# Optimization experiments

Hardware: AMD Instinct MI355X
Metric: run time of the kernel (lower is better)

## Reference

```python
import jax, jax.numpy as jnp
import numpy as np

F, H, K, T, IT, S = 128, 128, 768, 4, 2, 57  # feat, hidden, max_child, edge types, iters, num_sem


def setup_inputs() -> dict:
    key = jax.random.key(0)
    ks = jax.random.split(key, 12)

    def w(k, shape):
        fan = shape[0] if len(shape) == 2 else shape[1]
        return jax.random.normal(k, shape, jnp.float32) * fan ** -0.5

    return {
        "parent_feature": jax.random.normal(ks[0], (1, F), jnp.float32),
        "W_parent": w(ks[1], (F, H * K)), "b_parent": jnp.zeros((H * K,), jnp.float32),
        "W_exists": w(ks[2], (H, 1)), "b_exists": jnp.zeros((1,), jnp.float32),
        "W_edge_lat": w(ks[3], (2 * H, H)), "b_edge_lat": jnp.zeros((H,), jnp.float32),
        "W_edge_ex": w(ks[4], (T, H)), "b_edge_ex": jnp.zeros((T,), jnp.float32),
        "W_ne": w(ks[5], (IT, 2 * H, H)), "b_ne": jnp.zeros((IT, H), jnp.float32),
        "W_child": w(ks[6], (H * (IT + 1), H)), "b_child": jnp.zeros((H,), jnp.float32),
        "W_sem": w(ks[7], (H, S)), "b_sem": jnp.zeros((S,), jnp.float32),
        "W_child2": w(ks[8], (H, F)), "b_child2": jnp.zeros((F,), jnp.float32),
    }


def reference(parent_feature, W_parent, b_parent, W_exists, b_exists,
              W_edge_lat, b_edge_lat, W_edge_ex, b_edge_ex,
              W_ne, b_ne, W_child, b_child, W_sem, b_sem, W_child2, b_child2):
    # parent -> K child latents
    x = jax.nn.relu(parent_feature @ W_parent + b_parent)  # [1, K*H]
    cf = x.reshape(1, K, H)                                 # child feats
    exists_logits = cf @ W_exists + b_exists                # [1, K, 1]

    # pairwise edge latents [1, K, K, 2H] -> [1, K, K, H]
    pair0 = jnp.concatenate([
        jnp.broadcast_to(cf[:, :, None, :], (1, K, K, H)),
        jnp.broadcast_to(cf[:, None, :, :], (1, K, K, H))], axis=3)
    elat = jax.nn.relu(pair0 @ W_edge_lat + b_edge_lat)
    edge_logits = jnp.einsum('bijh,th->bijt', elat, W_edge_ex) + b_edge_ex  # [1,K,K,T]

    # fixed edge set: existing edges between existing nodes (dense mask form)
    exists = exists_logits[0, :, 0] > 0                     # [K]
    emask = jnp.any(edge_logits[0] > 0, axis=-1) & exists[:, None] & exists[None, :]
    any_edge = jnp.any(emask)

    feats = [cf]
    for i in range(IT):
        c = cf[0]                                           # [K, H]
        pair = jnp.concatenate([
            jnp.broadcast_to(c[:, None, :], (K, K, H)),
            jnp.broadcast_to(c[None, :, :], (K, K, H))], axis=2)
        msg = jax.nn.relu(pair @ W_ne[i] + b_ne[i])         # [K, K, H], >= 0
        msg = jnp.where(emask[:, :, None], msg, 0.0)
        # scatter_max with zeros-initialized out == max over masked neighbors (msg >= 0)
        new_cf = msg.max(axis=1)[None]                      # [1, K, H]
        cf = jnp.where(any_edge, new_cf, cf)                # no edges -> feats unchanged
        feats.append(cf)

    h = jnp.concatenate(feats, axis=2).reshape(K, H * (IT + 1))
    h = jax.nn.relu(h @ W_child + b_child)                  # [K, H]
    sem_logits = (h @ W_sem + b_sem).reshape(1, K, S)
    child_out = jax.nn.relu(h @ W_child2 + b_child2).reshape(1, K, F)
    return child_out, sem_logits, exists_logits, edge_logits
```

## Files before the change

### kernel.cpp

```cpp
#include <hip/hip_runtime.h>
#include <hip/hip_bf16.h>


#define NK 768
#define NH 128
#define NCF 98304

typedef float v2f __attribute__((ext_vector_type(2)));

__global__ __launch_bounds__(512) void k_pd(const float* __restrict__ pf,
    const float* __restrict__ Wp, const float* __restrict__ bp,
    const float* __restrict__ Wexi, const float* __restrict__ bexi,
    const float* __restrict__ Wel, const float* __restrict__ bel,
    const float* __restrict__ Wne, const float* __restrict__ Wee,
    float* __restrict__ cf0g, float* __restrict__ exO,
    float* __restrict__ A_T, float* __restrict__ BT,
    float* __restrict__ A0, float* __restrict__ B0,
    float* __restrict__ WeeT, unsigned int* __restrict__ flag)
{
    __shared__ float s_pf[128];
    __shared__ float s_cf0[2][128];
    __shared__ __align__(16) char s_scr[16384];
    int t = threadIdx.x;
    int b = blockIdx.x;
    int k0 = 2 * b;
    if (t < 128) s_pf[t] = pf[t];
    if (b == 0 && t == 0) *flag = 0u;
    if (b == 0) WeeT[(t & 127) * 4 + (t >> 7)] = Wee[t];
    __syncthreads();
    {
        float4* s_part = (float4*)s_scr;
        int c = t & 63, g = t >> 6;
        const float4* W4 = (const float4*)Wp;
        size_t base = (size_t)b * 64 + c;
        float4 acc = make_float4(0.f, 0.f, 0.f, 0.f);
        #pragma unroll
        for (int q = 0; q < 16; ++q) {
            int f = g * 16 + q;
            float4 w = W4[(size_t)f * 24576 + base];
            float p = s_pf[f];
            acc.x = fmaf(p, w.x, acc.x);
            acc.y = fmaf(p, w.y, acc.y);
            acc.z = fmaf(p, w.z, acc.z);
            acc.w = fmaf(p, w.w, acc.w);
        }
        s_part[g * 64 + c] = acc;
        __syncthreads();
        if (t < 64) {
            float4 r = s_part[t];
            #pragma unroll
            for (int g2 = 1; g2 < 8; ++g2) {
                float4 p = s_part[g2 * 64 + t];
                r.x += p.x; r.y += p.y; r.z += p.z; r.w += p.w;
            }
            float4 bi = ((const float4*)bp)[b * 64 + t];
            r.x = fmaxf(r.x + bi.x, 0.f);
            r.y = fmaxf(r.y + bi.y, 0.f);
            r.z = fmaxf(r.z + bi.z, 0.f);
            r.w = fmaxf(r.w + bi.w, 0.f);
            int row = t >> 5, h4 = t & 31;
            *(float4*)&s_cf0[row][h4 * 4] = r;
            ((float4*)cf0g)[(size_t)b * 64 + t] = r;
            float4 w = ((const float4*)Wexi)[h4];
            float dot = r.x * w.x + r.y * w.y + r.z * w.z + r.w * w.w;
            dot += __shfl_xor(dot, 16);
            dot += __shfl_xor(dot, 8);
            dot += __shfl_xor(dot, 4);
            dot += __shfl_xor(dot, 2);
            dot += __shfl_xor(dot, 1);
            if (h4 == 0) exO[k0 + row] = dot + bexi[0];
        }
    }
    __syncthreads();
    {
        float4* s_p2 = (float4*)s_scr;
        int mat = t >> 7, q = (t >> 5) & 3, c = t & 31;
        const float* W = (mat == 0) ? Wel : (mat == 1) ? (Wel + 16384)
                       : (mat == 2) ? Wne : (Wne + 16384);
        float4 a0 = make_float4(0.f, 0.f, 0.f, 0.f);
        float4 a1 = make_float4(0.f, 0.f, 0.f, 0.f);
        #pragma unroll 8
        for (int x = q * 32; x < q * 32 + 32; ++x) {
            float4 w = *(const float4*)&W[x * 128 + c * 4];
            float c0 = s_cf0[0][x], c1 = s_cf0[1][x];
            a0.x = fmaf(c0, w.x, a0.x); a0.y = fmaf(c0, w.y, a0.y);
            a0.z = fmaf(c0, w.z, a0.z); a0.w = fmaf(c0, w.w, a0.w);
            a1.x = fmaf(c1, w.x, a1.x); a1.y = fmaf(c1, w.y, a1.y);
            a1.z = fmaf(c1, w.z, a1.z); a1.w = fmaf(c1, w.w, a1.w);
        }
        s_p2[((mat * 4 + q) * 2 + 0) * 32 + c] = a0;
        s_p2[((mat * 4 + q) * 2 + 1) * 32 + c] = a1;
        __syncthreads();
        if (t < 256) {
            int m2 = t >> 6, row = (t >> 5) & 1, c2 = t & 31;
            float4 r = s_p2[((m2 * 4 + 0) * 2 + row) * 32 + c2];
            #pragma unroll
            for (int q2 = 1; q2 < 4; ++q2) {
                float4 p = s_p2[((m2 * 4 + q2) * 2 + row) * 32 + c2];
                r.x += p.x; r.y += p.y; r.z += p.z; r.w += p.w;
            }
            if (m2 == 0) {
                float4 bl = *(const float4*)&bel[c2 * 4];
                A_T[(size_t)(c2 * 4 + 0) * NK + k0 + row] = r.x + bl.x;
                A_T[(size_t)(c2 * 4 + 1) * NK + k0 + row] = r.y + bl.y;
                A_T[(size_t)(c2 * 4 + 2) * NK + k0 + row] = r.z + bl.z;
                A_T[(size_t)(c2 * 4 + 3) * NK + k0 + row] = r.w + bl.w;
            } else if (m2 == 1) {
                BT[(c2 * 4 + 0) * NK + k0 + row] = r.x;
                BT[(c2 * 4 + 1) * NK + k0 + row] = r.y;
                BT[(c2 * 4 + 2) * NK + k0 + row] = r.z;
                BT[(c2 * 4 + 3) * NK + k0 + row] = r.w;
            } else if (m2 == 2) {
                ((float4*)A0)[(size_t)(k0 + row) * 32 + c2] = r;
            } else {
                ((float4*)B0)[(size_t)(k0 + row) * 32 + c2] = r;
            }
        }
    }
}

__global__ __launch_bounds__(256) void k_edge(const float* __restrict__ A_T,
    const float* __restrict__ BT, const float* __restrict__ WeeT,
    const float* __restrict__ bex, const float* __restrict__ exO,
    float* __restrict__ edge_out, unsigned char* __restrict__ mask,
    unsigned int* __restrict__ flag)
{
    __shared__ float s_B[2][16][256];
    __shared__ float s_exi[4];
    __shared__ unsigned int s_any;
    int t = threadIdx.x;
    int i0 = blockIdx.x * 4;
    int j = blockIdx.y * 256 + t;
    float exj = exO[j];
    if (t < 4) s_exi[t] = exO[i0 + t];
    if (t == 0) s_any = 0u;
    const float4* BT4 = (const float4*)BT;
    int row = t >> 6, col = t & 63;
    {
        #pragma unroll
        for (int k = 0; k < 4; ++k)
            *(float4*)&s_B[0][row + k * 4][col * 4] =
                BT4[(size_t)(row + k * 4) * 192 + blockIdx.y * 64 + col];
    }
    __syncthreads();
    v2f l01[4] = {}, l23[4] = {};
    for (int c = 0; c < 8; ++c) {
        float4 r0, r1, r2, r3;
        if (c < 7) {
            size_t base = (size_t)((c + 1) * 16 + row) * 192 + blockIdx.y * 64 + col;
            r0 = BT4[base];
            r1 = BT4[base + 4 * 192];
            r2 = BT4[base + 8 * 192];
            r3 = BT4[base + 12 * 192];
        }
        int buf = c & 1;
        #pragma unroll
        for (int hh = 0; hh < 16; ++hh) {
            int h = c * 16 + hh;
            float4 av = *(const float4*)&A_T[(size_t)h * NK + i0];
            float4 wv = *(const float4*)&WeeT[h * 4];
            float bv = s_B[buf][hh][t];
            v2f e01 = __builtin_elementwise_max((v2f){av.x + bv, av.y + bv}, (v2f){0.f, 0.f});
            v2f e23 = __builtin_elementwise_max((v2f){av.z + bv, av.w + bv}, (v2f){0.f, 0.f});
            l01[0] += e01 * wv.x; l01[1] += e01 * wv.y;
            l01[2] += e01 * wv.z; l01[3] += e01 * wv.w;
            l23[0] += e23 * wv.x; l23[1] += e23 * wv.y;
            l23[2] += e23 * wv.z; l23[3] += e23 * wv.w;
        }
        if (c < 7) {
            int nb = (c + 1) & 1;
            *(float4*)&s_B[nb][row + 0][col * 4] = r0;
            *(float4*)&s_B[nb][row + 4][col * 4] = r1;
            *(float4*)&s_B[nb][row + 8][col * 4] = r2;
            *(float4*)&s_B[nb][row + 12][col * 4] = r3;
        }
        __syncthreads();
    }
    float b0 = bex[0], b1 = bex[1], b2 = bex[2], b3 = bex[3];
    bool ej = exj > 0.f;
    float4 v0 = make_float4(l01[0].x + b0, l01[1].x + b1, l01[2].x + b2, l01[3].x + b3);
    float4 v1 = make_float4(l01[0].y + b0, l01[1].y + b1, l01[2].y + b2, l01[3].y + b3);
    float4 v2 = make_float4(l23[0].x + b0, l23[1].x + b1, l23[2].x + b2, l23[3].x + b3);
    float4 v3 = make_float4(l23[0].y + b0, l23[1].y + b1, l23[2].y + b2, l23[3].y + b3);
    ((float4*)edge_out)[(size_t)(i0 + 0) * NK + j] = v0;
    ((float4*)edge_out)[(size_t)(i0 + 1) * NK + j] = v1;
    ((float4*)edge_out)[(size_t)(i0 + 2) * NK + j] = v2;
    ((float4*)edge_out)[(size_t)(i0 + 3) * NK + j] = v3;
    bool m0 = ((v0.x > 0.f) | (v0.y > 0.f) | (v0.z > 0.f) | (v0.w > 0.f)) && ej && (s_exi[0] > 0.f);
    bool m1 = ((v1.x > 0.f) | (v1.y > 0.f) | (v1.z > 0.f) | (v1.w > 0.f)) && ej && (s_exi[1] > 0.f);
    bool m2 = ((v2.x > 0.f) | (v2.y > 0.f) | (v2.z > 0.f) | (v2.w > 0.f)) && ej && (s_exi[2] > 0.f);
    bool m3 = ((v3.x > 0.f) | (v3.y > 0.f) | (v3.z > 0.f) | (v3.w > 0.f)) && ej && (s_exi[3] > 0.f);
    mask[(i0 + 0) * NK + j] = m0 ? (unsigned char)1 : (unsigned char)0;
    mask[(i0 + 1) * NK + j] = m1 ? (unsigned char)1 : (unsigned char)0;
    mask[(i0 + 2) * NK + j] = m2 ? (unsigned char)1 : (unsigned char)0;
    mask[(i0 + 3) * NK + j] = m3 ? (unsigned char)1 : (unsigned char)0;
    unsigned long long bal = __ballot((m0 | m1 | m2 | m3) ? 1 : 0);
    if ((t & 63) == 0 && bal) s_any = 1u;
    __syncthreads();
    if (t == 0 && s_any) *flag = 1u;
}

__global__ __launch_bounds__(512) void k_msgA(const float* __restrict__ B0,
    const unsigned char* __restrict__ mask, const float* __restrict__ A0,
    const float* __restrict__ bne, const float* __restrict__ cf0,
    const unsigned int* __restrict__ flag, float* __restrict__ cf1,
    const float* __restrict__ Wne1, float* __restrict__ A1, float* __restrict__ B1)
{
    __shared__ float s_madd[2][768];
    __shared__ float s_red[2][512];
    __shared__ float s_cf[2][128];
    int t = threadIdx.x;
    int k0 = blockIdx.x * 2;
    for (int idx = t; idx < 1536; idx += 512) {
        int r = idx >= 768 ? 1 : 0, jj = idx - r * 768;
        s_madd[r][jj] = mask[(k0 + r) * NK + jj] ? 0.f : -1e30f;
    }
    __syncthreads();
    int h = t & 127, q = t >> 7;
    float M0 = -1e30f, M1 = -1e30f;
    const float* bp2 = B0 + (size_t)q * 192 * 128 + h;
    const float* ma0 = &s_madd[0][q * 192];
    const float* ma1 = &s_madd[1][q * 192];
    #pragma unroll 16
    for (int jj = 0; jj < 192; ++jj) {
        float b = bp2[jj * 128];
        M0 = fmaxf(M0, b + ma0[jj]);
        M1 = fmaxf(M1, b + ma1[jj]);
    }
    s_red[0][t] = M0;
    s_red[1][t] = M1;
    __syncthreads();
    unsigned int fl = *flag;
    if (t < 256) {
        int kk = t >> 7, hh = t & 127;
        float M = fmaxf(fmaxf(s_red[kk][hh], s_red[kk][128 + hh]),
                        fmaxf(s_red[kk][256 + hh], s_red[kk][384 + hh]));
        int g = (k0 + kk) * 128 + hh;
        float v = fl ? fmaxf(A0[g] + bne[hh] + M, 0.f) : cf0[g];
        s_cf[kk][hh] = v;
        cf1[g] = v;
    }
    __syncthreads();
    int kk = (t >> 7) & 1, half = t >> 8;
    const float* W = Wne1 + half * 16384;
    const float* c = &s_cf[kk][0];
    float acc = 0.f;
    #pragma unroll 8
    for (int r = 0; r < 128; ++r)
        acc = fmaf(c[r], W[r * 128 + h], acc);
    float* D = half ? B1 : A1;
    D[(k0 + kk) * 128 + h] = acc;
}

__global__ __launch_bounds__(512) void k_finalf(const float* __restrict__ B1,
    const unsigned char* __restrict__ mask, const float* __restrict__ cf0,
    const float* __restrict__ cf1, const float* __restrict__ A1,
    const float* __restrict__ bne1, const unsigned int* __restrict__ flag,
    const float* __restrict__ Wc, const float* __restrict__ bc,
    const float* __restrict__ Wsem, const float* __restrict__ bsem,
    const float* __restrict__ W2, const float* __restrict__ b2,
    float* __restrict__ out)
{
    __shared__ float s_madd[2][768];
    __shared__ float s_red[2][512];
    __shared__ float s_M[2][128];
    __shared__ float s_f[2][384];
    __shared__ float s_h[2][128];
    __shared__ float s_hp[2][128];
    int t = threadIdx.x;
    int k0 = blockIdx.x * 2;
    for (int idx = t; idx < 1536; idx += 512) {
        int r = idx >= 768 ? 1 : 0, jj = idx - r * 768;
        s_madd[r][jj] = mask[(k0 + r) * NK + jj] ? 0.f : -1e30f;
    }
    __syncthreads();
    int h = t & 127, q = t >> 7;
    {
        float M0 = -1e30f, M1 = -1e30f;
        const float* bp2 = B1 + (size_t)q * 192 * 128 + h;
        const float* ma0 = &s_madd[0][q * 192];
        const float* ma1 = &s_madd[1][q * 192];
        #pragma unroll 16
        for (int jj = 0; jj < 192; ++jj) {
            float b = bp2[jj * 128];
            M0 = fmaxf(M0, b + ma0[jj]);
            M1 = fmaxf(M1, b + ma1[jj]);
        }
        s_red[0][t] = M0;
        s_red[1][t] = M1;
    }
    __syncthreads();
    if (t < 256) {
        int kk = t >> 7, hh = t & 127;
        s_M[kk][hh] = fmaxf(fmaxf(s_red[kk][hh], s_red[kk][128 + hh]),
                            fmaxf(s_red[kk][256 + hh], s_red[kk][384 + hh]));
    }
    __syncthreads();
    unsigned int fl = *flag;
    for (int idx = t; idx < 768; idx += 512) {
        int kk = idx >= 384 ? 1 : 0;
        int c = idx - kk * 384;
        int row = k0 + kk;
        float v;
        if (c < 128) v = cf0[row * 128 + c];
        else if (c < 256) v = cf1[row * 128 + (c - 128)];
        else {
            int hh = c - 256, g = row * 128 + hh;
            v = fl ? fmaxf(A1[g] + bne1[hh] + s_M[kk][hh], 0.f) : cf1[g];
        }
        s_f[kk][c] = v;
    }
    __syncthreads();
    int rh = (t >> 7) & 1, kg = t >> 8;
    float acc = 0.f;
    {
        const float* f = &s_f[kg][rh * 192];
        const float* Wcp = Wc + rh * 192 * 128;
        #pragma unroll 8
        for (int r = 0; r < 192; ++r)
            acc = fmaf(f[r], Wcp[r * 128 + h], acc);
    }
    if (rh) s_hp[kg][h] = acc;
    __syncthreads();
    if (!rh) s_h[kg][h] = fmaxf(acc + s_hp[kg][h] + bc[h], 0.f);
    __syncthreads();
    float a2 = 0.f;
    {
        const float* hr = &s_h[kg][rh * 64];
        const float* W2p = W2 + rh * 64 * 128;
        #pragma unroll 8
        for (int r = 0; r < 64; ++r)
            a2 = fmaf(hr[r], W2p[r * 128 + h], a2);
    }
    if (rh) s_hp[kg][h] = a2;
    __syncthreads();
    if (!rh) out[(size_t)(k0 + kg) * 128 + h] = fmaxf(a2 + s_hp[kg][h] + b2[h], 0.f);
    if (t < 114) {
        int kk = t / 57, sidx = t - kk * 57;
        float ss = bsem[sidx];
        const float* hr = &s_h[kk][0];
        #pragma unroll 8
        for (int r = 0; r < 128; ++r)
            ss = fmaf(hr[r], Wsem[r * 57 + sidx], ss);
        out[98304 + (size_t)(k0 + kk) * 57 + sidx] = ss;
    }
}

extern "C" void kernel_launch(void* const* d_in, const int* in_sizes, int n_in,
                              void* d_out, int out_size, void* d_ws, size_t ws_size,
                              hipStream_t stream) {
    const float* pf   = (const float*)d_in[0];
    const float* Wp   = (const float*)d_in[1];
    const float* bp   = (const float*)d_in[2];
    const float* Wexi = (const float*)d_in[3];
    const float* bexi = (const float*)d_in[4];
    const float* Wel  = (const float*)d_in[5];
    const float* bel  = (const float*)d_in[6];
    const float* Wee  = (const float*)d_in[7];
    const float* bee  = (const float*)d_in[8];
    const float* Wne  = (const float*)d_in[9];
    const float* bne  = (const float*)d_in[10];
    const float* Wc   = (const float*)d_in[11];
    const float* bc   = (const float*)d_in[12];
    const float* Wsem = (const float*)d_in[13];
    const float* bsem = (const float*)d_in[14];
    const float* W2   = (const float*)d_in[15];
    const float* b2   = (const float*)d_in[16];
    float* out = (float*)d_out;
    float* ws  = (float*)d_ws;
    const int N = NCF;
    float* cf0 = ws;
    float* cf1 = ws + N;
    float* A_T = ws + 2 * N;
    float* BT  = ws + 3 * N;
    float* A0  = ws + 4 * N;
    float* B0  = ws + 5 * N;
    float* A1  = ws + 6 * N;
    float* B1  = ws + 7 * N;
    float* WeeT = ws + 8 * N;
    unsigned char* mask = (unsigned char*)(ws + 8 * N + 512);
    unsigned int* flag  = (unsigned int*)(mask + 589824);

    float* out_ex   = out + 142080;
    float* out_edge = out + 142848;

    k_pd<<<384, 512, 0, stream>>>(pf, Wp, bp, Wexi, bexi, Wel, bel, Wne, Wee,
                                  cf0, out_ex, A_T, BT, A0, B0, WeeT, flag);
    k_edge<<<dim3(192, 3), 256, 0, stream>>>(A_T, BT, WeeT, bee, out_ex,
                                             out_edge, mask, flag);
    k_msgA<<<384, 512, 0, stream>>>(B0, mask, A0, bne, cf0, flag, cf1,
                                    Wne + 32768, A1, B1);
    k_finalf<<<384, 512, 0, stream>>>(B1, mask, cf0, cf1, A1, bne + 128, flag,
                                      Wc, bc, Wsem, bsem, W2, b2, out);
}
```

Measured before the change: 76.16 us.

## Fuse edge-logit kernel with first message-passing iteration

Merges the edge logit/mask kernel into the first message kernel. Each block computes edge logits for two parent rows across all children, builds the mask directly in shared memory and then performs the masked max reduction. The no-edge fallback moves to the final kernel so the fused kernel no longer waits on the global flag. This removes a launch and the mask round trip through global memory. In exchange it changes the edge-compute tiling to fewer rows per block and uses larger shared buffers, which may lower reuse and occupancy.

Result: slower. 113.8 us (+49.4%).

```diff
diff --git a/kernel.cpp b/kernel.cpp
--- a/kernel.cpp
+++ b/kernel.cpp
@@ -119,137 +119,135 @@
     }
 }
 
-__global__ __launch_bounds__(256) void k_edge(const float* __restrict__ A_T,
+__global__ __launch_bounds__(512) void k_em(const float* __restrict__ A_T,
     const float* __restrict__ BT, const float* __restrict__ WeeT,
     const float* __restrict__ bex, const float* __restrict__ exO,
+    const float* __restrict__ B0, const float* __restrict__ A0,
+    const float* __restrict__ bne,
     float* __restrict__ edge_out, unsigned char* __restrict__ mask,
-    unsigned int* __restrict__ flag)
-{
-    __shared__ float s_B[2][16][256];
-    __shared__ float s_exi[4];
-    __shared__ unsigned int s_any;
-    int t = threadIdx.x;
-    int i0 = blockIdx.x * 4;
-    int j = blockIdx.y * 256 + t;
-    float exj = exO[j];
-    if (t < 4) s_exi[t] = exO[i0 + t];
-    if (t == 0) s_any = 0u;
-    const float4* BT4 = (const float4*)BT;
-    int row = t >> 6, col = t & 63;
-    {
-        #pragma unroll
-        for (int k = 0; k < 4; ++k)
-            *(float4*)&s_B[0][row + k * 4][col * 4] =
-                BT4[(size_t)(row + k * 4) * 192 + blockIdx.y * 64 + col];
-    }
-    __syncthreads();
-    v2f l01[4] = {}, l23[4] = {};
-    for (int c = 0; c < 8; ++c) {
-        float4 r0, r1, r2, r3;
-        if (c < 7) {
-            size_t base = (size_t)((c + 1) * 16 + row) * 192 + blockIdx.y * 64 + col;
-            r0 = BT4[base];
-            r1 = BT4[base + 4 * 192];
-            r2 = BT4[base + 8 * 192];
-            r3 = BT4[base + 12 * 192];
-        }
-        int buf = c & 1;
-        #pragma unroll
-        for (int hh = 0; hh < 16; ++hh) {
-            int h = c * 16 + hh;
-            float4 av = *(const float4*)&A_T[(size_t)h * NK + i0];
-            float4 wv = *(const float4*)&WeeT[h * 4];
-            float bv = s_B[buf][hh][t];
-            v2f e01 = __builtin_elementwise_max((v2f){av.x + bv, av.y + bv}, (v2f){0.f, 0.f});
-            v2f e23 = __builtin_elementwise_max((v2f){av.z + bv, av.w + bv}, (v2f){0.f, 0.f});
-            l01[0] += e01 * wv.x; l01[1] += e01 * wv.y;
-            l01[2] += e01 * wv.z; l01[3] += e01 * wv.w;
-            l23[0] += e23 * wv.x; l23[1] += e23 * wv.y;
-            l23[2] += e23 * wv.z; l23[3] += e23 * wv.w;
-        }
-        if (c < 7) {
-            int nb = (c + 1) & 1;
-            *(float4*)&s_B[nb][row + 0][col * 4] = r0;
-            *(float4*)&s_B[nb][row + 4][col * 4] = r1;
-            *(float4*)&s_B[nb][row + 8][col * 4] = r2;
-            *(float4*)&s_B[nb][row + 12][col * 4] = r3;
-        }
-        __syncthreads();
-    }
-    float b0 = bex[0], b1 = bex[1], b2 = bex[2], b3 = bex[3];
-    bool ej = exj > 0.f;
-    float4 v0 = make_float4(l01[0].x + b0, l01[1].x + b1, l01[2].x + b2, l01[3].x + b3);
-    float4 v1 = make_float4(l01[0].y + b0, l01[1].y + b1, l01[2].y + b2, l01[3].y + b3);
-    float4 v2 = make_float4(l23[0].x + b0, l23[1].x + b1, l23[2].x + b2, l23[3].x + b3);
-    float4 v3 = make_float4(l23[0].y + b0, l23[1].y + b1, l23[2].y + b2, l23[3].y + b3);
-    ((float4*)edge_out)[(size_t)(i0 + 0) * NK + j] = v0;
-    ((float4*)edge_out)[(size_t)(i0 + 1) * NK + j] = v1;
-    ((float4*)edge_out)[(size_t)(i0 + 2) * NK + j] = v2;
-    ((float4*)edge_out)[(size_t)(i0 + 3) * NK + j] = v3;
-    bool m0 = ((v0.x > 0.f) | (v0.y > 0.f) | (v0.z > 0.f) | (v0.w > 0.f)) && ej && (s_exi[0] > 0.f);
-    bool m1 = ((v1.x > 0.f) | (v1.y > 0.f) | (v1.z > 0.f) | (v1.w > 0.f)) && ej && (s_exi[1] > 0.f);
-    bool m2 = ((v2.x > 0.f) | (v2.y > 0.f) | (v2.z > 0.f) | (v2.w > 0.f)) && ej && (s_exi[2] > 0.f);
-    bool m3 = ((v3.x > 0.f) | (v3.y > 0.f) | (v3.z > 0.f) | (v3.w > 0.f)) && ej && (s_exi[3] > 0.f);
-    mask[(i0 + 0) * NK + j] = m0 ? (unsigned char)1 : (unsigned char)0;
-    mask[(i0 + 1) * NK + j] = m1 ? (unsigned char)1 : (unsigned char)0;
-    mask[(i0 + 2) * NK + j] = m2 ? (unsigned char)1 : (unsigned char)0;
-    mask[(i0 + 3) * NK + j] = m3 ? (unsigned char)1 : (unsigned char)0;
-    unsigned long long bal = __ballot((m0 | m1 | m2 | m3) ? 1 : 0);
-    if ((t & 63) == 0 && bal) s_any = 1u;
-    __syncthreads();
-    if (t == 0 && s_any) *flag = 1u;
-}
-
-__global__ __launch_bounds__(512) void k_msgA(const float* __restrict__ B0,
-    const unsigned char* __restrict__ mask, const float* __restrict__ A0,
-    const float* __restrict__ bne, const float* __restrict__ cf0,
-    const unsigned int* __restrict__ flag, float* __restrict__ cf1,
+    unsigned int* __restrict__ flag, float* __restrict__ cf1,
     const float* __restrict__ Wne1, float* __restrict__ A1, float* __restrict__ B1)
 {
+    __shared__ float s_B[2][8][768];
     __shared__ float s_madd[2][768];
     __shared__ float s_red[2][512];
     __shared__ float s_cf[2][128];
+    __shared__ unsigned int s_any;
     int t = threadIdx.x;
-    int k0 = blockIdx.x * 2;
-    for (int idx = t; idx < 1536; idx += 512) {
-        int r = idx >= 768 ? 1 : 0, jj = idx - r * 768;
-        s_madd[r][jj] = mask[(k0 + r) * NK + jj] ? 0.f : -1e30f;
-    }
-    __syncthreads();
+    int i0 = blockIdx.x * 2;
+    if (t == 0) s_any = 0u;
+    bool two = t < 256;
+    int j0 = t;
+    int j1 = two ? t + 512 : t;
+    float ex0 = exO[j0];
+    float ex1 = exO[j1];
+    float exi0 = exO[i0], exi1 = exO[i0 + 1];
+    const float4* BT4 = (const float4*)BT;
+    float4 pre[3];
+    #pragma unroll
+    for (int k = 0; k < 3; ++k) {
+        int idx = t + k * 512;
+        pre[k] = BT4[(size_t)(idx / 192) * 192 + (idx % 192)];
+    }
+    v2f l0[4] = {}, l1[4] = {};
+    for (int ch = 0; ch < 16; ++ch) {
+        int buf = ch & 1;
+        #pragma unroll
+        for (int k = 0; k < 3; ++k)
+            ((float4*)&s_B[buf][0][0])[t + k * 512] = pre[k];
+        __syncthreads();
+        if (ch < 15) {
+            #pragma unroll
+            for (int k = 0; k < 3; ++k) {
+                int idx = t + k * 512;
+                pre[k] = BT4[(size_t)((ch + 1) * 8 + idx / 192) * 192 + (idx % 192)];
+            }
+        }
+        #pragma unroll
+        for (int hh = 0; hh < 8; ++hh) {
+            int h = ch * 8 + hh;
+            float2 av = *(const float2*)&A_T[(size_t)h * NK + i0];
+            float4 wv = *(const float4*)&WeeT[h * 4];
+            v2f bv = { s_B[buf][hh][j0], s_B[buf][hh][j1] };
+            v2f e0 = __builtin_elementwise_max(bv + (v2f){av.x, av.x}, (v2f){0.f, 0.f});
+            v2f e1 = __builtin_elementwise_max(bv + (v2f){av.y, av.y}, (v2f){0.f, 0.f});
+            l0[0] += e0 * (v2f){wv.x, wv.x}; l0[1] += e0 * (v2f){wv.y, wv.y};
+            l0[2] += e0 * (v2f){wv.z, wv.z}; l0[3] += e0 * (v2f){wv.w, wv.w};
+            l1[0] += e1 * (v2f){wv.x, wv.x}; l1[1] += e1 * (v2f){wv.y, wv.y};
+            l1[2] += e1 * (v2f){wv.z, wv.z}; l1[3] += e1 * (v2f){wv.w, wv.w};
+        }
+    }
+    float b0 = bex[0], b1 = bex[1], b2 = bex[2], b3 = bex[3];
+    float4* eo = (float4*)edge_out;
+    float4 v00 = make_float4(l0[0].x + b0, l0[1].x + b1, l0[2].x + b2, l0[3].x + b3);
+    float4 v10 = make_float4(l1[0].x + b0, l1[1].x + b1, l1[2].x + b2, l1[3].x + b3);
+    eo[(size_t)(i0 + 0) * NK + j0] = v00;
+    eo[(size_t)(i0 + 1) * NK + j0] = v10;
+    bool m00 = ((v00.x > 0.f) | (v00.y > 0.f) | (v00.z > 0.f) | (v00.w > 0.f))
+               && (ex0 > 0.f) && (exi0 > 0.f);
+    bool m10 = ((v10.x > 0.f) | (v10.y > 0.f) | (v10.z > 0.f) | (v10.w > 0.f))
+               && (ex0 > 0.f) && (exi1 > 0.f);
+    s_madd[0][j0] = m00 ? 0.f : -1e30f;
+    s_madd[1][j0] = m10 ? 0.f : -1e30f;
+    mask[(i0 + 0) * NK + j0] = m00 ? (unsigned char)1 : (unsigned char)0;
+    mask[(i0 + 1) * NK + j0] = m10 ? (unsigned char)1 : (unsigned char)0;
+    bool anyL = m00 | m10;
+    if (two) {
+        float4 v01 = make_float4(l0[0].y + b0, l0[1].y + b1, l0[2].y + b2, l0[3].y + b3);
+        float4 v11 = make_float4(l1[0].y + b0, l1[1].y + b1, l1[2].y + b2, l1[3].y + b3);
+        eo[(size_t)(i0 + 0) * NK + j1] = v01;
+        eo[(size_t)(i0 + 1) * NK + j1] = v11;
+        bool m01 = ((v01.x > 0.f) | (v01.y > 0.f) | (v01.z > 0.f) | (v01.w > 0.f))
+                   && (ex1 > 0.f) && (exi0 > 0.f);
+        bool m11 = ((v11.x > 0.f) | (v11.y > 0.f) | (v11.z > 0.f) | (v11.w > 0.f))
+                   && (ex1 > 0.f) && (exi1 > 0.f);
+        s_madd[0][j1] = m01 ? 0.f : -1e30f;
+        s_madd[1][j1] = m11 ? 0.f : -1e30f;
+        mask[(i0 + 0) * NK + j1] = m01 ? (unsigned char)1 : (unsigned char)0;
+        mask[(i0 + 1) * NK + j1] = m11 ? (unsigned char)1 : (unsigned char)0;
+        anyL |= m01 | m11;
+    }
+    unsigned long long bal = __ballot(anyL ? 1 : 0);
+    if ((t & 63) == 0 && bal) s_any = 1u;
+    __syncthreads();
+    if (t == 0 && s_any) *flag = 1u;
     int h = t & 127, q = t >> 7;
-    float M0 = -1e30f, M1 = -1e30f;
-    const float* bp2 = B0 + (size_t)q * 192 * 128 + h;
-    const float* ma0 = &s_madd[0][q * 192];
-    const float* ma1 = &s_madd[1][q * 192];
-    #pragma unroll 16
-    for (int jj = 0; jj < 192; ++jj) {
-        float b = bp2[jj * 128];
-        M0 = fmaxf(M0, b + ma0[jj]);
-        M1 = fmaxf(M1, b + ma1[jj]);
-    }
-    s_red[0][t] = M0;
-    s_red[1][t] = M1;
-    __syncthreads();
-    unsigned int fl = *flag;
+    {
+        float M0 = -1e30f, M1 = -1e30f;
+        const float* bp2 = B0 + (size_t)q * 192 * 128 + h;
+        const float* ma0 = &s_madd[0][q * 192];
+        const float* ma1 = &s_madd[1][q * 192];
+        #pragma unroll 16
+        for (int jj = 0; jj < 192; ++jj) {
+            float bb = bp2[jj * 128];
+            M0 = fmaxf(M0, bb + ma0[jj]);
+            M1 = fmaxf(M1, bb + ma1[jj]);
+        }
+        s_red[0][t] = M0;
+        s_red[1][t] = M1;
+    }
+    __syncthreads();
     if (t < 256) {
         int kk = t >> 7, hh = t & 127;
         float M = fmaxf(fmaxf(s_red[kk][hh], s_red[kk][128 + hh]),
                         fmaxf(s_red[kk][256 + hh], s_red[kk][384 + hh]));
-        int g = (k0 + kk) * 128 + hh;
-        float v = fl ? fmaxf(A0[g] + bne[hh] + M, 0.f) : cf0[g];
+        int g = (i0 + kk) * 128 + hh;
+        float v = fmaxf(A0[g] + bne[hh] + M, 0.f);
         s_cf[kk][hh] = v;
         cf1[g] = v;
     }
     __syncthreads();
-    int kk = (t >> 7) & 1, half = t >> 8;
-    const float* W = Wne1 + half * 16384;
-    const float* c = &s_cf[kk][0];
-    float acc = 0.f;
-    #pragma unroll 8
-    for (int r = 0; r < 128; ++r)
-        acc = fmaf(c[r], W[r * 128 + h], acc);
-    float* D = half ? B1 : A1;
-    D[(k0 + kk) * 128 + h] = acc;
+    {
+        int kk = (t >> 7) & 1, half = t >> 8;
+        const float* W = Wne1 + half * 16384;
+        const float* c = &s_cf[kk][0];
+        float acc = 0.f;
+        #pragma unroll 8
+        for (int r = 0; r < 128; ++r)
+            acc = fmaf(c[r], W[r * 128 + h], acc);
+        float* D = half ? B1 : A1;
+        D[(i0 + kk) * 128 + h] = acc;
+    }
 }
 
 __global__ __launch_bounds__(512) void k_finalf(const float* __restrict__ B1,
@@ -303,10 +301,10 @@
         int row = k0 + kk;
         float v;
         if (c < 128) v = cf0[row * 128 + c];
-        else if (c < 256) v = cf1[row * 128 + (c - 128)];
+        else if (c < 256) v = fl ? cf1[row * 128 + (c - 128)] : cf0[row * 128 + (c - 128)];
         else {
             int hh = c - 256, g = row * 128 + hh;
-            v = fl ? fmaxf(A1[g] + bne1[hh] + s_M[kk][hh], 0.f) : cf1[g];
+            v = fl ? fmaxf(A1[g] + bne1[hh] + s_M[kk][hh], 0.f) : cf0[g];
         }
         s_f[kk][c] = v;
     }
@@ -386,10 +384,8 @@
 
     k_pd<<<384, 512, 0, stream>>>(pf, Wp, bp, Wexi, bexi, Wel, bel, Wne, Wee,
                                   cf0, out_ex, A_T, BT, A0, B0, WeeT, flag);
-    k_edge<<<dim3(192, 3), 256, 0, stream>>>(A_T, BT, WeeT, bee, out_ex,
-                                             out_edge, mask, flag);
-    k_msgA<<<384, 512, 0, stream>>>(B0, mask, A0, bne, cf0, flag, cf1,
-                                    Wne + 32768, A1, B1);
+    k_em<<<384, 512, 0, stream>>>(A_T, BT, WeeT, bee, out_ex, B0, A0, bne,
+                                  out_edge, mask, flag, cf1, Wne + 32768, A1, B1);
     k_finalf<<<384, 512, 0, stream>>>(B1, mask, cf0, cf1, A1, bne + 128, flag,
                                       Wc, bc, Wsem, bsem, W2, b2, out);
 }
```
